# Performance work log

Hardware: AMD Instinct MI355X
Metric: run time of the kernel (lower is better)

## Reference

```python
import jax, jax.numpy as jnp
import numpy as np

N, E, IN_FEATS, HID, HEADS = 50000, 800000, 256, 32, 8
NEG_SLOPE = 0.2


def _init_params(key):
    ks = jax.random.split(key, 12)
    def lin(k, fi, fo):
        return jax.random.normal(k, (fi, fo), jnp.float32) * (1.0 / np.sqrt(fi))
    p = {}
    # layer 0: in_feats -> HID x HEADS
    p['W0'] = lin(ks[0], IN_FEATS, HEADS * HID)
    p['al0'] = jax.random.normal(ks[1], (HEADS, HID), jnp.float32) * 0.1
    p['ar0'] = jax.random.normal(ks[2], (HEADS, HID), jnp.float32) * 0.1
    p['b0'] = jnp.zeros((HEADS * HID,), jnp.float32)
    # layer 1: HID*HEADS -> HID x HEADS
    p['W1'] = lin(ks[3], HEADS * HID, HEADS * HID)
    p['al1'] = jax.random.normal(ks[4], (HEADS, HID), jnp.float32) * 0.1
    p['ar1'] = jax.random.normal(ks[5], (HEADS, HID), jnp.float32) * 0.1
    p['b1'] = jnp.zeros((HEADS * HID,), jnp.float32)
    # layer 2 (final): HID*HEADS -> HID x 1 head, no activation
    p['W2'] = lin(ks[6], HEADS * HID, HID)
    p['al2'] = jax.random.normal(ks[7], (1, HID), jnp.float32) * 0.1
    p['ar2'] = jax.random.normal(ks[8], (1, HID), jnp.float32) * 0.1
    p['b2'] = jnp.zeros((HID,), jnp.float32)
    return p


def setup_inputs() -> dict:
    key = jax.random.key(0)
    k1, k2, k3, kp = jax.random.split(key, 4)
    inp = {
        'features': jax.random.normal(k1, (N, IN_FEATS), jnp.float32),
        'src': jax.random.randint(k2, (E,), 0, N, jnp.int32),
        'dst': jax.random.randint(k3, (E,), 0, N, jnp.int32),
    }
    inp.update(_init_params(kp))
    return inp


def _gat_layer(x, src, dst, W, al, ar, b, heads, act):
    n = x.shape[0]
    d = W.shape[1] // heads
    feat = (x @ W).reshape(n, heads, d)           # [N,H,D]
    el = jnp.sum(feat * al, axis=-1)              # [N,H]
    er = jnp.sum(feat * ar, axis=-1)              # [N,H]
    e = jax.nn.leaky_relu(el[src] + er[dst], NEG_SLOPE)   # [E,H]
    # segment softmax over destination neighborhoods
    emax = jax.ops.segment_max(e, dst, num_segments=n)
    ex = jnp.exp(e - emax[dst])
    denom = jax.ops.segment_sum(ex, dst, num_segments=n)
    a = ex / (denom[dst] + 1e-9)                  # [E,H]
    msg = feat[src] * a[:, :, None]               # [E,H,D]
    out = jax.ops.segment_sum(msg, dst, num_segments=n)   # [N,H,D]
    out = out + b.reshape(1, heads, d)
    return act(out) if act is not None else out


def reference(features, src, dst, W0, al0, ar0, b0, W1, al1, ar1, b1, W2, al2, ar2, b2):
    h = _gat_layer(features, src, dst, W0, al0, ar0, b0, HEADS, jax.nn.elu)
    h = h.reshape(h.shape[0], -1)
    h = _gat_layer(h, src, dst, W1, al1, ar1, b1, HEADS, jax.nn.elu)
    h = h.reshape(h.shape[0], -1)
    h = _gat_layer(h, src, dst, W2, al2, ar2, b2, 1, None)   # [N,1,D]
    return h.mean(axis=1)                                    # [N,D]
```

## Files before the change

kernel.cpp:

```cpp
#include <hip/hip_runtime.h>

typedef unsigned short u16;
typedef unsigned int   u32;
typedef __attribute__((ext_vector_type(8))) short  short8;
typedef __attribute__((ext_vector_type(4))) float  f32x4;
typedef __attribute__((ext_vector_type(2))) float  f32x2;
typedef __attribute__((ext_vector_type(2))) unsigned int u32v2;

#define NN 50000
#define NE 800000

__device__ __forceinline__ float bf2f(u16 b) { return __uint_as_float(((u32)b) << 16); }
__device__ __forceinline__ float bflo(u32 p) { return __uint_as_float(p << 16); }
__device__ __forceinline__ float bfhi(u32 p) { return __uint_as_float(p & 0xffff0000u); }
__device__ __forceinline__ u16 f2bf(float f) {
    u32 u = __float_as_uint(f);
    u32 r = u + 0x7fffu + ((u >> 16) & 1u);
    return (u16)(r >> 16);
}
__device__ __forceinline__ float lexp(float v) {
    v = v > 0.f ? v : 0.2f * v;
    return __expf(fminf(v, 60.f));
}

struct DetectArgs { const u32* p[13]; int nw[13]; };

__global__ void k_detect(DetectArgs a, int* flags) {
    int t = threadIdx.x;
    if (t >= 13) return;
    const u32* x = a.p[t];
    int n = a.nw[t];
    int hits = 0, nz = 0;
    for (int i = 0; i < n; ++i) {
        u32 w = x[i];
        if (!w) continue;
        ++nz;
        u32 e = (w >> 7) & 0xffu;
        if (e >= 100 && e <= 150) ++hits;
    }
    flags[t] = (nz == 0) ? 2 : ((hits * 2 >= nz) ? 0 : 1);
}

struct ConvArgs { const void* s[9]; float* d[9]; int n[9]; int fi[9]; };

__global__ void k_convert(ConvArgs a, const int* __restrict__ flags) {
    int j = blockIdx.y;
    int i = blockIdx.x * 256 + threadIdx.x;
    if (i >= a.n[j]) return;
    int fl = flags[a.fi[j]];
    float v = 0.f;
    if (fl == 1) v = ((const float*)a.s[j])[i];
    else if (fl == 0) v = bf2f(((const u16*)a.s[j])[i]);
    a.d[j][i] = v;
}

__global__ void k_wpack(const void* __restrict__ Wsrc, const int* __restrict__ flags,
                        int fidx, int N, u16* __restrict__ Wp, int nchunks) {
    int id = blockIdx.x * 256 + threadIdx.x;
    if (id >= nchunks) return;
    int L = id & 63, kt = (id >> 6) & 7, nt = id >> 9;
    int col = nt * 16 + (L & 15);
    int krow = kt * 32 + ((L >> 4) & 3) * 8;
    bool isf32 = (flags[fidx] == 1);
#pragma unroll
    for (int j = 0; j < 8; ++j) {
        int s = (krow + j) * N + col;
        Wp[id * 8 + j] = isf32 ? f2bf(((const float*)Wsrc)[s]) : ((const u16*)Wsrc)[s];
    }
}

__global__ void k_xprep(const void* __restrict__ X, const int* __restrict__ flag,
                        u32* __restrict__ Xb2, int total2) {
    int i = blockIdx.x * 256 + threadIdx.x;
    if (i >= total2) return;
    if (*flag == 1) {
        const float* Xf = (const float*)X;
        Xb2[i] = (u32)f2bf(Xf[2 * i]) | ((u32)f2bf(Xf[2 * i + 1]) << 16);
    } else {
        Xb2[i] = ((const u32*)X)[i];
    }
}

__global__ void k_hist(const int* __restrict__ dst, int* __restrict__ deg, int E) {
    int e = blockIdx.x * 256 + threadIdx.x;
    if (e < E) atomicAdd(&deg[dst[e]], 1);
}

__global__ __launch_bounds__(256) void k_scan_partial(const int* __restrict__ deg,
                                                      int* __restrict__ bsum, int n) {
    __shared__ int red[256];
    int t = threadIdx.x;
    int i = blockIdx.x * 256 + t;
    red[t] = (i < n) ? deg[i] : 0;
    __syncthreads();
    for (int ofs = 128; ofs > 0; ofs >>= 1) {
        if (t < ofs) red[t] += red[t + ofs];
        __syncthreads();
    }
    if (t == 0) bsum[blockIdx.x] = red[0];
}

__global__ __launch_bounds__(256) void k_scan_bsum(int* __restrict__ bsum, int nb) {
    __shared__ int s[256];
    int t = threadIdx.x;
    int v = (t < nb) ? bsum[t] : 0;
    s[t] = v;
    __syncthreads();
    for (int ofs = 1; ofs < 256; ofs <<= 1) {
        int x = (t >= ofs) ? s[t - ofs] : 0;
        __syncthreads();
        s[t] += x;
        __syncthreads();
    }
    if (t < nb) bsum[t] = s[t] - v;
}

__global__ __launch_bounds__(256) void k_scan_final(const int* __restrict__ deg,
                                                    const int* __restrict__ bsum,
                                                    int* __restrict__ rowptr,
                                                    int* __restrict__ cursor, int n) {
    __shared__ int s[256];
    int t = threadIdx.x;
    int i = blockIdx.x * 256 + t;
    int v = (i < n) ? deg[i] : 0;
    s[t] = v;
    __syncthreads();
    for (int ofs = 1; ofs < 256; ofs <<= 1) {
        int x = (t >= ofs) ? s[t - ofs] : 0;
        __syncthreads();
        s[t] += x;
        __syncthreads();
    }
    int excl = bsum[blockIdx.x] + s[t] - v;
    if (i < n) {
        rowptr[i] = excl;
        cursor[i] = excl;
        if (i == n - 1) rowptr[n] = excl + v;
    }
}

__global__ void k_scatter(const int* __restrict__ src, const int* __restrict__ dst,
                          int* __restrict__ cursor, int* __restrict__ csr_src, int E) {
    int e = blockIdx.x * 256 + threadIdx.x;
    if (e >= E) return;
    int p = atomicAdd(&cursor[dst[e]], 1);
    csr_src[p] = src[e];
}

__global__ __launch_bounds__(256) void k_gemm_mfma(const u16* __restrict__ Xb,
                                                   const u16* __restrict__ Wp,
                                                   u16* __restrict__ OUT, int nrows) {
    __shared__ u16 As[64 * 256];
    const int t = threadIdx.x;
    const int w = t >> 6, L = t & 63;
    const int quad = (L >> 4) & 3;
    const int r0 = blockIdx.x * 64;
    const int nb = blockIdx.y * 8;

    const short8* Xv = (const short8*)Xb;
    short8* Asv = (short8*)As;
    short8 zero = {0, 0, 0, 0, 0, 0, 0, 0};
#pragma unroll
    for (int i = 0; i < 8; ++i) {
        int g = i * 256 + t;
        int row = g >> 5, cc = g & 31;
        int r = r0 + row;
        Asv[cc * 64 + row] = (r < nrows) ? Xv[(size_t)r * 32 + cc] : zero;
    }

    const short8* Wv = (const short8*)Wp;
    short8 bf[2][8];
#pragma unroll
    for (int jn = 0; jn < 2; ++jn) {
        int nt = nb + w + jn * 4;
#pragma unroll
        for (int kt = 0; kt < 8; ++kt) bf[jn][kt] = Wv[(nt * 8 + kt) * 64 + L];
    }
    __syncthreads();

    f32x4 acc[4][2];
#pragma unroll
    for (int mi = 0; mi < 4; ++mi)
#pragma unroll
        for (int jn = 0; jn < 2; ++jn) acc[mi][jn] = (f32x4){0.f, 0.f, 0.f, 0.f};

#pragma unroll
    for (int kt = 0; kt < 8; ++kt) {
#pragma unroll
        for (int mi = 0; mi < 4; ++mi) {
            short8 af = Asv[(kt * 4 + quad) * 64 + mi * 16 + (L & 15)];
            acc[mi][0] = __builtin_amdgcn_mfma_f32_16x16x32_bf16(af, bf[0][kt], acc[mi][0], 0, 0, 0);
            acc[mi][1] = __builtin_amdgcn_mfma_f32_16x16x32_bf16(af, bf[1][kt], acc[mi][1], 0, 0, 0);
        }
    }

    const int colbase = blockIdx.y * 128;
#pragma unroll
    for (int mi = 0; mi < 4; ++mi) {
        int rb = r0 + mi * 16 + quad * 4;
#pragma unroll
        for (int jn = 0; jn < 2; ++jn) {
            int c = colbase + (w + jn * 4) * 16 + (L & 15);
#pragma unroll
            for (int reg = 0; reg < 4; ++reg) {
                int r = rb + reg;
                if (r < nrows) OUT[(size_t)r * 256 + c] = f2bf(acc[mi][jn][reg]);
            }
        }
    }
}

__global__ __launch_bounds__(256) void k_gemm_mfma32(const u16* __restrict__ Xb,
                                                     const u16* __restrict__ Wp,
                                                     u16* __restrict__ OUT, int nrows) {
    __shared__ u16 As[128 * 256];
    const int t = threadIdx.x;
    const int w = t >> 6, L = t & 63;
    const int quad = (L >> 4) & 3;
    const int r0 = blockIdx.x * 128;
    const int mh = (w >> 1) * 64, nt = w & 1;

    const short8* Xv = (const short8*)Xb;
    short8* Asv = (short8*)As;
    short8 zero = {0, 0, 0, 0, 0, 0, 0, 0};
#pragma unroll
    for (int i = 0; i < 16; ++i) {
        int g = i * 256 + t;
        int row = g >> 5, cc = g & 31;
        int r = r0 + row;
        Asv[cc * 128 + row] = (r < nrows) ? Xv[(size_t)r * 32 + cc] : zero;
    }

    const short8* Wv = (const short8*)Wp;
    short8 bf[8];
#pragma unroll
    for (int kt = 0; kt < 8; ++kt) bf[kt] = Wv[(nt * 8 + kt) * 64 + L];
    __syncthreads();

    f32x4 acc[4];
#pragma unroll
    for (int mi = 0; mi < 4; ++mi) acc[mi] = (f32x4){0.f, 0.f, 0.f, 0.f};

#pragma unroll
    for (int kt = 0; kt < 8; ++kt) {
#pragma unroll
        for (int mi = 0; mi < 4; ++mi) {
            short8 af = Asv[(kt * 4 + quad) * 128 + mh + mi * 16 + (L & 15)];
            acc[mi] = __builtin_amdgcn_mfma_f32_16x16x32_bf16(af, bf[kt], acc[mi], 0, 0, 0);
        }
    }

#pragma unroll
    for (int mi = 0; mi < 4; ++mi) {
        int rb = r0 + mh + mi * 16 + quad * 4;
        int c = nt * 16 + (L & 15);
#pragma unroll
        for (int reg = 0; reg < 4; ++reg) {
            int r = rb + reg;
            if (r < nrows) OUT[(size_t)r * 32 + c] = f2bf(acc[mi][reg]);
        }
    }
}

__global__ void k_elr8(const u16* __restrict__ featb, const float* __restrict__ al,
                       const float* __restrict__ ar, float* __restrict__ el,
                       float* __restrict__ er, int n) {
    int idx = blockIdx.x * 256 + threadIdx.x;
    if (idx >= n * 8) return;
    int node = idx >> 3, h = idx & 7;
    const u32* fu = (const u32*)featb + (size_t)node * 128 + h * 16;
    const float* A = al + h * 32;
    const float* B = ar + h * 32;
    float sl = 0.f, sr = 0.f;
#pragma unroll
    for (int j = 0; j < 16; ++j) {
        u32 w = fu[j];
        float f0 = bflo(w), f1 = bfhi(w);
        sl += f0 * A[2 * j] + f1 * A[2 * j + 1];
        sr += f0 * B[2 * j] + f1 * B[2 * j + 1];
    }
    el[idx] = sl;
    er[idx] = sr;
}

__global__ void k_elr1(const u16* __restrict__ featb, const float* __restrict__ al,
                       const float* __restrict__ ar, float* __restrict__ el,
                       float* __restrict__ er, int n) {
    int node = blockIdx.x * 256 + threadIdx.x;
    if (node >= n) return;
    const u32* fu = (const u32*)featb + (size_t)node * 16;
    float sl = 0.f, sr = 0.f;
#pragma unroll
    for (int j = 0; j < 16; ++j) {
        u32 w = fu[j];
        float f0 = bflo(w), f1 = bfhi(w);
        sl += f0 * al[2 * j] + f1 * al[2 * j + 1];
        sr += f0 * ar[2 * j] + f1 * ar[2 * j + 1];
    }
    el[node] = sl;
    er[node] = sr;
}

__global__ __launch_bounds__(256) void k_gather8(const int* __restrict__ rowptr,
                                                 const int* __restrict__ csr_src,
                                                 const float* __restrict__ el,
                                                 const float* __restrict__ er,
                                                 const u32v2* __restrict__ featb4,
                                                 const float* __restrict__ bias,
                                                 u32v2* __restrict__ xout4) {
    int t = threadIdx.x;
    int d = blockIdx.x * 4 + (t >> 6);
    int q = t & 63;
    int h = q >> 3;
    int b = rowptr[d], e = rowptr[d + 1];
    float erd = er[d * 8 + h];
    float a0 = 0.f, a1 = 0.f, a2 = 0.f, a3 = 0.f, ssum = 0.f;
    int p = b;
    for (; p + 4 <= e; p += 4) {
        int s0 = csr_src[p], s1 = csr_src[p + 1], s2 = csr_src[p + 2], s3 = csr_src[p + 3];
        float e0 = lexp(el[s0 * 8 + h] + erd);
        float e1 = lexp(el[s1 * 8 + h] + erd);
        float e2 = lexp(el[s2 * 8 + h] + erd);
        float e3 = lexp(el[s3 * 8 + h] + erd);
        u32v2 w0 = featb4[(size_t)s0 * 64 + q];
        u32v2 w1 = featb4[(size_t)s1 * 64 + q];
        u32v2 w2 = featb4[(size_t)s2 * 64 + q];
        u32v2 w3 = featb4[(size_t)s3 * 64 + q];
        a0 += bflo(w0.x) * e0; a1 += bfhi(w0.x) * e0; a2 += bflo(w0.y) * e0; a3 += bfhi(w0.y) * e0;
        a0 += bflo(w1.x) * e1; a1 += bfhi(w1.x) * e1; a2 += bflo(w1.y) * e1; a3 += bfhi(w1.y) * e1;
        a0 += bflo(w2.x) * e2; a1 += bfhi(w2.x) * e2; a2 += bflo(w2.y) * e2; a3 += bfhi(w2.y) * e2;
        a0 += bflo(w3.x) * e3; a1 += bfhi(w3.x) * e3; a2 += bflo(w3.y) * e3; a3 += bfhi(w3.y) * e3;
        ssum += (e0 + e1) + (e2 + e3);
    }
    for (; p < e; ++p) {
        int s = csr_src[p];
        float ev = lexp(el[s * 8 + h] + erd);
        u32v2 w = featb4[(size_t)s * 64 + q];
        a0 += bflo(w.x) * ev; a1 += bfhi(w.x) * ev;
        a2 += bflo(w.y) * ev; a3 += bfhi(w.y) * ev;
        ssum += ev;
    }
    float rd = 1.f / (ssum + 1e-9f);
    const float4 bb = *(const float4*)&bias[4 * q];
    float v0 = a0 * rd + bb.x;
    float v1 = a1 * rd + bb.y;
    float v2 = a2 * rd + bb.z;
    float v3 = a3 * rd + bb.w;
    v0 = v0 > 0.f ? v0 : expm1f(v0);
    v1 = v1 > 0.f ? v1 : expm1f(v1);
    v2 = v2 > 0.f ? v2 : expm1f(v2);
    v3 = v3 > 0.f ? v3 : expm1f(v3);
    u32v2 o;
    o.x = (u32)f2bf(v0) | ((u32)f2bf(v1) << 16);
    o.y = (u32)f2bf(v2) | ((u32)f2bf(v3) << 16);
    xout4[(size_t)d * 64 + q] = o;
}

__global__ __launch_bounds__(256) void k_gather1(const int* __restrict__ rowptr,
                                                 const int* __restrict__ csr_src,
                                                 const float* __restrict__ el,
                                                 const float* __restrict__ er,
                                                 const u32* __restrict__ featb2,
                                                 const float* __restrict__ bias,
                                                 void* __restrict__ out,
                                                 const int* __restrict__ flag, int n) {
    int t = threadIdx.x;
    int d = blockIdx.x * 16 + (t >> 4);
    int q = t & 15;
    if (d >= n) return;
    int b = rowptr[d], e = rowptr[d + 1];
    float erd = er[d];
    float a0 = 0.f, a1 = 0.f, ssum = 0.f;
    int p = b;
    for (; p + 4 <= e; p += 4) {
        int s0 = csr_src[p], s1 = csr_src[p + 1], s2 = csr_src[p + 2], s3 = csr_src[p + 3];
        float e0 = lexp(el[s0] + erd);
        float e1 = lexp(el[s1] + erd);
        float e2 = lexp(el[s2] + erd);
        float e3 = lexp(el[s3] + erd);
        u32 w0 = featb2[(size_t)s0 * 16 + q];
        u32 w1 = featb2[(size_t)s1 * 16 + q];
        u32 w2 = featb2[(size_t)s2 * 16 + q];
        u32 w3 = featb2[(size_t)s3 * 16 + q];
        a0 += bflo(w0) * e0; a1 += bfhi(w0) * e0;
        a0 += bflo(w1) * e1; a1 += bfhi(w1) * e1;
        a0 += bflo(w2) * e2; a1 += bfhi(w2) * e2;
        a0 += bflo(w3) * e3; a1 += bfhi(w3) * e3;
        ssum += (e0 + e1) + (e2 + e3);
    }
    for (; p < e; ++p) {
        int s = csr_src[p];
        float ev = lexp(el[s] + erd);
        u32 w = featb2[(size_t)s * 16 + q];
        a0 += bflo(w) * ev;
        a1 += bfhi(w) * ev;
        ssum += ev;
    }
    float rd = 1.f / (ssum + 1e-9f);
    float v0 = a0 * rd + bias[2 * q];
    float v1 = a1 * rd + bias[2 * q + 1];
    if (*flag == 1) {
        f32x2 o = {v0, v1};
        ((f32x2*)out)[(size_t)d * 16 + q] = o;
    } else {
        ((u32*)out)[(size_t)d * 16 + q] = (u32)f2bf(v0) | ((u32)f2bf(v1) << 16);
    }
}

extern "C" void kernel_launch(void* const* d_in, const int* in_sizes, int n_in,
                              void* d_out, int out_size, void* d_ws, size_t ws_size,
                              hipStream_t stream) {
    const void* features = d_in[0];
    const int* src = (const int*)d_in[1];
    const int* dst = (const int*)d_in[2];

    char* ws = (char*)d_ws;
    size_t off = 0;
    auto carve = [&](size_t bytes) -> void* {
        void* p = ws + off;
        off = (off + bytes + 255) & ~(size_t)255;
        return p;
    };
    int*   flags = (int*)carve(64);
    float* pconv = (float*)carve(2048 * 4);
    u16*   Wp0 = (u16*)carve(65536 * 2);
    u16*   Wp1 = (u16*)carve(65536 * 2);
    u16*   Wp2 = (u16*)carve(8192 * 2);
    u16*   Xb    = (u16*)carve((size_t)NN * 256 * 2);
    u16*   featb = (u16*)carve((size_t)NN * 256 * 2);
    float* el   = (float*)carve((size_t)NN * 8 * 4);
    float* er   = (float*)carve((size_t)NN * 8 * 4);
    int*   deg     = (int*)carve((size_t)NN * 4);
    int*   cursor  = (int*)carve((size_t)NN * 4);
    int*   rowptr  = (int*)carve((size_t)(NN + 1) * 4);
    int*   bsum    = (int*)carve(256 * 4);
    int*   csr_src = (int*)carve((size_t)NE * 4);
    if (off > ws_size) return;

    const int N = NN, E = NE;
    const int nscan = (N + 255) / 256;

    DetectArgs da;
    const int din_idx[13] = {0, 3, 4, 5, 6, 7, 8, 9, 10, 11, 12, 13, 14};
    for (int j = 0; j < 13; ++j) {
        da.p[j] = (const u32*)d_in[din_idx[j]];
        int nw = in_sizes[din_idx[j]] / 2;
        da.nw[j] = nw > 512 ? 512 : nw;
    }
    k_detect<<<1, 64, 0, stream>>>(da, flags);

    ConvArgs ca;
    const int psl[9] = {4, 5, 6, 8, 9, 10, 12, 13, 14};
    const int pfl[9] = {2, 3, 4, 6, 7, 8, 10, 11, 12};
    float* dsts[9];
    {
        size_t o = 0;
        for (int j = 0; j < 9; ++j) {
            dsts[j] = pconv + o;
            o += (size_t)in_sizes[psl[j]];
        }
    }
    for (int j = 0; j < 9; ++j) {
        ca.s[j] = d_in[psl[j]];
        ca.d[j] = dsts[j];
        ca.n[j] = in_sizes[psl[j]];
        ca.fi[j] = pfl[j];
    }
    k_convert<<<dim3(1, 9), 256, 0, stream>>>(ca, flags);
    float* al0f = dsts[0]; float* ar0f = dsts[1]; float* b0f = dsts[2];
    float* al1f = dsts[3]; float* ar1f = dsts[4]; float* b1f = dsts[5];
    float* al2f = dsts[6]; float* ar2f = dsts[7]; float* b2f = dsts[8];

    k_wpack<<<32, 256, 0, stream>>>(d_in[3],  flags, 1, 256, Wp0, 8192);
    k_wpack<<<32, 256, 0, stream>>>(d_in[7],  flags, 5, 256, Wp1, 8192);
    k_wpack<<<4,  256, 0, stream>>>(d_in[11], flags, 9, 32,  Wp2, 1024);

    k_xprep<<<(N * 128 + 255) / 256, 256, 0, stream>>>(features, flags, (u32*)Xb, N * 128);

    hipMemsetAsync(deg, 0, (size_t)N * 4, stream);
    k_hist<<<(E + 255) / 256, 256, 0, stream>>>(dst, deg, E);
    k_scan_partial<<<nscan, 256, 0, stream>>>(deg, bsum, N);
    k_scan_bsum<<<1, 256, 0, stream>>>(bsum, nscan);
    k_scan_final<<<nscan, 256, 0, stream>>>(deg, bsum, rowptr, cursor, N);
    k_scatter<<<(E + 255) / 256, 256, 0, stream>>>(src, dst, cursor, csr_src, E);

    const dim3 ggrid((N + 63) / 64, 2);

    k_gemm_mfma<<<ggrid, 256, 0, stream>>>(Xb, Wp0, featb, N);
    k_elr8<<<(N * 8 + 255) / 256, 256, 0, stream>>>(featb, al0f, ar0f, el, er, N);
    k_gather8<<<N / 4, 256, 0, stream>>>(rowptr, csr_src, el, er,
                                         (const u32v2*)featb, b0f, (u32v2*)Xb);

    k_gemm_mfma<<<ggrid, 256, 0, stream>>>(Xb, Wp1, featb, N);
    k_elr8<<<(N * 8 + 255) / 256, 256, 0, stream>>>(featb, al1f, ar1f, el, er, N);
    k_gather8<<<N / 4, 256, 0, stream>>>(rowptr, csr_src, el, er,
                                         (const u32v2*)featb, b1f, (u32v2*)Xb);

    k_gemm_mfma32<<<(N + 127) / 128, 256, 0, stream>>>(Xb, Wp2, featb, N);
    k_elr1<<<(N + 255) / 256, 256, 0, stream>>>(featb, al2f, ar2f, el, er, N);
    k_gather1<<<(N + 15) / 16, 256, 0, stream>>>(rowptr, csr_src, el, er,
                                                 (const u32*)featb, b2f,
                                                 d_out, flags, N);
}
```

Measured before the change: 493.9 us.

## Fuse fp32-to-bf16 input conversion into GEMM and widen gather to 16B lanes

Removes the separate k_xprep pass: the first GEMM now reads fp32 features directly and converts them to bf16 while staging into LDS. This drops a full write and re-read of the converted feature matrix. The 8-head gather kernel now handles two destination nodes per wave, with each lane loading 16 bytes (8 bf16 values) instead of 8. Its loop runs to the larger degree of the two nodes and masks out the extra edges, which may waste work when the two degrees differ.

```diff
diff --git a/kernel.cpp b/kernel.cpp
--- a/kernel.cpp
+++ b/kernel.cpp
@@ -6,6 +6,7 @@
 typedef __attribute__((ext_vector_type(4))) float  f32x4;
 typedef __attribute__((ext_vector_type(2))) float  f32x2;
 typedef __attribute__((ext_vector_type(2))) unsigned int u32v2;
+typedef __attribute__((ext_vector_type(4))) unsigned int u32v4;
 
 #define NN 50000
 #define NE 800000
@@ -66,18 +67,6 @@
     for (int j = 0; j < 8; ++j) {
         int s = (krow + j) * N + col;
         Wp[id * 8 + j] = isf32 ? f2bf(((const float*)Wsrc)[s]) : ((const u16*)Wsrc)[s];
-    }
-}
-
-__global__ void k_xprep(const void* __restrict__ X, const int* __restrict__ flag,
-                        u32* __restrict__ Xb2, int total2) {
-    int i = blockIdx.x * 256 + threadIdx.x;
-    if (i >= total2) return;
-    if (*flag == 1) {
-        const float* Xf = (const float*)X;
-        Xb2[i] = (u32)f2bf(Xf[2 * i]) | ((u32)f2bf(Xf[2 * i + 1]) << 16);
-    } else {
-        Xb2[i] = ((const u32*)X)[i];
     }
 }
 
@@ -147,7 +136,8 @@
     csr_src[p] = src[e];
 }
 
-__global__ __launch_bounds__(256) void k_gemm_mfma(const u16* __restrict__ Xb,
+__global__ __launch_bounds__(256) void k_gemm_mfma(const void* __restrict__ Xv,
+                                                   const int* __restrict__ xflag,
                                                    const u16* __restrict__ Wp,
                                                    u16* __restrict__ OUT, int nrows) {
     __shared__ u16 As[64 * 256];
@@ -156,8 +146,8 @@
     const int quad = (L >> 4) & 3;
     const int r0 = blockIdx.x * 64;
     const int nb = blockIdx.y * 8;
-
-    const short8* Xv = (const short8*)Xb;
+    const bool xf32 = (xflag != nullptr) && (*xflag == 1);
+
     short8* Asv = (short8*)As;
     short8 zero = {0, 0, 0, 0, 0, 0, 0, 0};
 #pragma unroll
@@ -165,7 +155,21 @@
         int g = i * 256 + t;
         int row = g >> 5, cc = g & 31;
         int r = r0 + row;
-        Asv[cc * 64 + row] = (r < nrows) ? Xv[(size_t)r * 32 + cc] : zero;
+        short8 val = zero;
+        if (r < nrows) {
+            if (xf32) {
+                const f32x4* Xf4 = (const f32x4*)Xv;
+                f32x4 lo = Xf4[(size_t)r * 64 + cc * 2];
+                f32x4 hi = Xf4[(size_t)r * 64 + cc * 2 + 1];
+                val[0] = (short)f2bf(lo[0]); val[1] = (short)f2bf(lo[1]);
+                val[2] = (short)f2bf(lo[2]); val[3] = (short)f2bf(lo[3]);
+                val[4] = (short)f2bf(hi[0]); val[5] = (short)f2bf(hi[1]);
+                val[6] = (short)f2bf(hi[2]); val[7] = (short)f2bf(hi[3]);
+            } else {
+                val = ((const short8*)Xv)[(size_t)r * 32 + cc];
+            }
+        }
+        Asv[cc * 64 + row] = val;
     }
 
     const short8* Wv = (const short8*)Wp;
@@ -305,55 +309,59 @@
                                                  const int* __restrict__ csr_src,
                                                  const float* __restrict__ el,
                                                  const float* __restrict__ er,
-                                                 const u32v2* __restrict__ featb4,
+                                                 const u32v4* __restrict__ featb4,
                                                  const float* __restrict__ bias,
-                                                 u32v2* __restrict__ xout4) {
+                                                 u32v4* __restrict__ xout4, int E) {
     int t = threadIdx.x;
-    int d = blockIdx.x * 4 + (t >> 6);
-    int q = t & 63;
-    int h = q >> 3;
+    int wave = t >> 6, lane = t & 63;
+    int half = lane >> 5, li = lane & 31;
+    int d = blockIdx.x * 8 + wave * 2 + half;
+    int q = li;
+    int h = q >> 2;
     int b = rowptr[d], e = rowptr[d + 1];
+    int deg = e - b;
+    int md = max(deg, __shfl_xor(deg, 32, 64));
     float erd = er[d * 8 + h];
-    float a0 = 0.f, a1 = 0.f, a2 = 0.f, a3 = 0.f, ssum = 0.f;
-    int p = b;
-    for (; p + 4 <= e; p += 4) {
-        int s0 = csr_src[p], s1 = csr_src[p + 1], s2 = csr_src[p + 2], s3 = csr_src[p + 3];
-        float e0 = lexp(el[s0 * 8 + h] + erd);
-        float e1 = lexp(el[s1 * 8 + h] + erd);
-        float e2 = lexp(el[s2 * 8 + h] + erd);
-        float e3 = lexp(el[s3 * 8 + h] + erd);
-        u32v2 w0 = featb4[(size_t)s0 * 64 + q];
-        u32v2 w1 = featb4[(size_t)s1 * 64 + q];
-        u32v2 w2 = featb4[(size_t)s2 * 64 + q];
-        u32v2 w3 = featb4[(size_t)s3 * 64 + q];
-        a0 += bflo(w0.x) * e0; a1 += bfhi(w0.x) * e0; a2 += bflo(w0.y) * e0; a3 += bfhi(w0.y) * e0;
-        a0 += bflo(w1.x) * e1; a1 += bfhi(w1.x) * e1; a2 += bflo(w1.y) * e1; a3 += bfhi(w1.y) * e1;
-        a0 += bflo(w2.x) * e2; a1 += bfhi(w2.x) * e2; a2 += bflo(w2.y) * e2; a3 += bfhi(w2.y) * e2;
-        a0 += bflo(w3.x) * e3; a1 += bfhi(w3.x) * e3; a2 += bflo(w3.y) * e3; a3 += bfhi(w3.y) * e3;
-        ssum += (e0 + e1) + (e2 + e3);
-    }
-    for (; p < e; ++p) {
-        int s = csr_src[p];
-        float ev = lexp(el[s * 8 + h] + erd);
-        u32v2 w = featb4[(size_t)s * 64 + q];
-        a0 += bflo(w.x) * ev; a1 += bfhi(w.x) * ev;
-        a2 += bflo(w.y) * ev; a3 += bfhi(w.y) * ev;
-        ssum += ev;
+    float a0 = 0.f, a1 = 0.f, a2 = 0.f, a3 = 0.f;
+    float a4 = 0.f, a5 = 0.f, a6 = 0.f, a7 = 0.f, ssum = 0.f;
+    for (int it = 0; it < md; it += 4) {
+#pragma unroll
+        for (int k = 0; k < 4; ++k) {
+            int p = b + it + k;
+            bool act = p < e;
+            int pc = min(p, E - 1);
+            int s = csr_src[pc];
+            float ev = lexp(el[s * 8 + h] + erd);
+            ev = act ? ev : 0.f;
+            u32v4 w = featb4[(size_t)s * 32 + q];
+            a0 += bflo(w.x) * ev; a1 += bfhi(w.x) * ev;
+            a2 += bflo(w.y) * ev; a3 += bfhi(w.y) * ev;
+            a4 += bflo(w.z) * ev; a5 += bfhi(w.z) * ev;
+            a6 += bflo(w.w) * ev; a7 += bfhi(w.w) * ev;
+            ssum += ev;
+        }
     }
     float rd = 1.f / (ssum + 1e-9f);
-    const float4 bb = *(const float4*)&bias[4 * q];
-    float v0 = a0 * rd + bb.x;
-    float v1 = a1 * rd + bb.y;
-    float v2 = a2 * rd + bb.z;
-    float v3 = a3 * rd + bb.w;
+    const float4 bb0 = *(const float4*)&bias[8 * q];
+    const float4 bb1 = *(const float4*)&bias[8 * q + 4];
+    float v0 = a0 * rd + bb0.x, v1 = a1 * rd + bb0.y;
+    float v2 = a2 * rd + bb0.z, v3 = a3 * rd + bb0.w;
+    float v4 = a4 * rd + bb1.x, v5 = a5 * rd + bb1.y;
+    float v6 = a6 * rd + bb1.z, v7 = a7 * rd + bb1.w;
     v0 = v0 > 0.f ? v0 : expm1f(v0);
     v1 = v1 > 0.f ? v1 : expm1f(v1);
     v2 = v2 > 0.f ? v2 : expm1f(v2);
     v3 = v3 > 0.f ? v3 : expm1f(v3);
-    u32v2 o;
+    v4 = v4 > 0.f ? v4 : expm1f(v4);
+    v5 = v5 > 0.f ? v5 : expm1f(v5);
+    v6 = v6 > 0.f ? v6 : expm1f(v6);
+    v7 = v7 > 0.f ? v7 : expm1f(v7);
+    u32v4 o;
     o.x = (u32)f2bf(v0) | ((u32)f2bf(v1) << 16);
     o.y = (u32)f2bf(v2) | ((u32)f2bf(v3) << 16);
-    xout4[(size_t)d * 64 + q] = o;
+    o.z = (u32)f2bf(v4) | ((u32)f2bf(v5) << 16);
+    o.w = (u32)f2bf(v6) | ((u32)f2bf(v7) << 16);
+    xout4[(size_t)d * 32 + q] = o;
 }
 
 __global__ __launch_bounds__(256) void k_gather1(const int* __restrict__ rowptr,
@@ -475,8 +483,6 @@
     k_wpack<<<32, 256, 0, stream>>>(d_in[7],  flags, 5, 256, Wp1, 8192);
     k_wpack<<<4,  256, 0, stream>>>(d_in[11], flags, 9, 32,  Wp2, 1024);
 
-    k_xprep<<<(N * 128 + 255) / 256, 256, 0, stream>>>(features, flags, (u32*)Xb, N * 128);
-
     hipMemsetAsync(deg, 0, (size_t)N * 4, stream);
     k_hist<<<(E + 255) / 256, 256, 0, stream>>>(dst, deg, E);
     k_scan_partial<<<nscan, 256, 0, stream>>>(deg, bsum, N);
@@ -486,15 +492,15 @@
 
     const dim3 ggrid((N + 63) / 64, 2);
 
-    k_gemm_mfma<<<ggrid, 256, 0, stream>>>(Xb, Wp0, featb, N);
+    k_gemm_mfma<<<ggrid, 256, 0, stream>>>(features, flags, Wp0, featb, N);
     k_elr8<<<(N * 8 + 255) / 256, 256, 0, stream>>>(featb, al0f, ar0f, el, er, N);
-    k_gather8<<<N / 4, 256, 0, stream>>>(rowptr, csr_src, el, er,
-                                         (const u32v2*)featb, b0f, (u32v2*)Xb);
-
-    k_gemm_mfma<<<ggrid, 256, 0, stream>>>(Xb, Wp1, featb, N);
+    k_gather8<<<N / 8, 256, 0, stream>>>(rowptr, csr_src, el, er,
+                                         (const u32v4*)featb, b0f, (u32v4*)Xb, E);
+
+    k_gemm_mfma<<<ggrid, 256, 0, stream>>>(Xb, nullptr, Wp1, featb, N);
     k_elr8<<<(N * 8 + 255) / 256, 256, 0, stream>>>(featb, al1f, ar1f, el, er, N);
-    k_gather8<<<N / 4, 256, 0, stream>>>(rowptr, csr_src, el, er,
-                                         (const u32v2*)featb, b1f, (u32v2*)Xb);
+    k_gather8<<<N / 8, 256, 0, stream>>>(rowptr, csr_src, el, er,
+                                         (const u32v4*)featb, b1f, (u32v4*)Xb, E);
 
     k_gemm_mfma32<<<(N + 127) / 128, 256, 0, stream>>>(Xb, Wp2, featb, N);
     k_elr1<<<(N + 255) / 256, 256, 0, stream>>>(featb, al2f, ar2f, el, er, N);
```

Measured after the change: 502.7 us. Within noise of the previous version (+1.8%).

## Fuse fp32-to-bf16 feature conversion into first GEMM and parallelize dtype detection

Applied to the files above, without the earlier changes.

Removes the separate feature-conversion kernel. The first MFMA GEMM now reads fp32 features directly and converts them to bf16 while staging tiles into shared memory, which avoids writing and re-reading a 25.6 MB bf16 copy. Dtype detection now uses one 256-thread block per tensor with a shared-memory reduction instead of one serial thread per tensor. The el/er kernels switch to 128-bit vector loads. The trade-off is a fp32 read path and a runtime flag branch inside the GEMM, plus the GEMM is launched with two column blocks, so it reads the fp32 features twice.

```diff
diff --git a/kernel.cpp b/kernel.cpp
--- a/kernel.cpp
+++ b/kernel.cpp
@@ -6,6 +6,7 @@
 typedef __attribute__((ext_vector_type(4))) float  f32x4;
 typedef __attribute__((ext_vector_type(2))) float  f32x2;
 typedef __attribute__((ext_vector_type(2))) unsigned int u32v2;
+typedef __attribute__((ext_vector_type(4))) unsigned int u32v4;
 
 #define NN 50000
 #define NE 800000
@@ -25,20 +26,28 @@
 
 struct DetectArgs { const u32* p[13]; int nw[13]; };
 
-__global__ void k_detect(DetectArgs a, int* flags) {
+__global__ __launch_bounds__(256) void k_detect(DetectArgs a, int* flags) {
+    __shared__ int sh[256], sz[256];
+    int j = blockIdx.x;
+    const u32* x = a.p[j];
+    int n = a.nw[j];
     int t = threadIdx.x;
-    if (t >= 13) return;
-    const u32* x = a.p[t];
-    int n = a.nw[t];
     int hits = 0, nz = 0;
-    for (int i = 0; i < n; ++i) {
+    for (int i = t; i < n; i += 256) {
         u32 w = x[i];
-        if (!w) continue;
-        ++nz;
-        u32 e = (w >> 7) & 0xffu;
-        if (e >= 100 && e <= 150) ++hits;
-    }
-    flags[t] = (nz == 0) ? 2 : ((hits * 2 >= nz) ? 0 : 1);
+        if (w) {
+            ++nz;
+            u32 e = (w >> 7) & 0xffu;
+            if (e >= 100 && e <= 150) ++hits;
+        }
+    }
+    sh[t] = hits; sz[t] = nz;
+    __syncthreads();
+    for (int ofs = 128; ofs > 0; ofs >>= 1) {
+        if (t < ofs) { sh[t] += sh[t + ofs]; sz[t] += sz[t + ofs]; }
+        __syncthreads();
+    }
+    if (t == 0) flags[j] = (sz[0] == 0) ? 2 : ((sh[0] * 2 >= sz[0]) ? 0 : 1);
 }
 
 struct ConvArgs { const void* s[9]; float* d[9]; int n[9]; int fi[9]; };
@@ -66,18 +75,6 @@
     for (int j = 0; j < 8; ++j) {
         int s = (krow + j) * N + col;
         Wp[id * 8 + j] = isf32 ? f2bf(((const float*)Wsrc)[s]) : ((const u16*)Wsrc)[s];
-    }
-}
-
-__global__ void k_xprep(const void* __restrict__ X, const int* __restrict__ flag,
-                        u32* __restrict__ Xb2, int total2) {
-    int i = blockIdx.x * 256 + threadIdx.x;
-    if (i >= total2) return;
-    if (*flag == 1) {
-        const float* Xf = (const float*)X;
-        Xb2[i] = (u32)f2bf(Xf[2 * i]) | ((u32)f2bf(Xf[2 * i + 1]) << 16);
-    } else {
-        Xb2[i] = ((const u32*)X)[i];
     }
 }
 
@@ -147,7 +144,8 @@
     csr_src[p] = src[e];
 }
 
-__global__ __launch_bounds__(256) void k_gemm_mfma(const u16* __restrict__ Xb,
+__global__ __launch_bounds__(256) void k_gemm_mfma(const void* __restrict__ Xv,
+                                                   const int* __restrict__ xflag,
                                                    const u16* __restrict__ Wp,
                                                    u16* __restrict__ OUT, int nrows) {
     __shared__ u16 As[64 * 256];
@@ -156,8 +154,8 @@
     const int quad = (L >> 4) & 3;
     const int r0 = blockIdx.x * 64;
     const int nb = blockIdx.y * 8;
-
-    const short8* Xv = (const short8*)Xb;
+    const bool xf32 = (xflag != nullptr) && (*xflag == 1);
+
     short8* Asv = (short8*)As;
     short8 zero = {0, 0, 0, 0, 0, 0, 0, 0};
 #pragma unroll
@@ -165,7 +163,21 @@
         int g = i * 256 + t;
         int row = g >> 5, cc = g & 31;
         int r = r0 + row;
-        Asv[cc * 64 + row] = (r < nrows) ? Xv[(size_t)r * 32 + cc] : zero;
+        short8 val = zero;
+        if (r < nrows) {
+            if (xf32) {
+                const f32x4* Xf4 = (const f32x4*)Xv;
+                f32x4 lo = Xf4[(size_t)r * 64 + cc * 2];
+                f32x4 hi = Xf4[(size_t)r * 64 + cc * 2 + 1];
+                val[0] = (short)f2bf(lo[0]); val[1] = (short)f2bf(lo[1]);
+                val[2] = (short)f2bf(lo[2]); val[3] = (short)f2bf(lo[3]);
+                val[4] = (short)f2bf(hi[0]); val[5] = (short)f2bf(hi[1]);
+                val[6] = (short)f2bf(hi[2]); val[7] = (short)f2bf(hi[3]);
+            } else {
+                val = ((const short8*)Xv)[(size_t)r * 32 + cc];
+            }
+        }
+        Asv[cc * 64 + row] = val;
     }
 
     const short8* Wv = (const short8*)Wp;
@@ -268,16 +280,21 @@
     int idx = blockIdx.x * 256 + threadIdx.x;
     if (idx >= n * 8) return;
     int node = idx >> 3, h = idx & 7;
-    const u32* fu = (const u32*)featb + (size_t)node * 128 + h * 16;
+    const u32v4* fu = (const u32v4*)((const u32*)featb + (size_t)node * 128 + h * 16);
     const float* A = al + h * 32;
     const float* B = ar + h * 32;
     float sl = 0.f, sr = 0.f;
 #pragma unroll
-    for (int j = 0; j < 16; ++j) {
-        u32 w = fu[j];
-        float f0 = bflo(w), f1 = bfhi(w);
-        sl += f0 * A[2 * j] + f1 * A[2 * j + 1];
-        sr += f0 * B[2 * j] + f1 * B[2 * j + 1];
+    for (int j = 0; j < 4; ++j) {
+        u32v4 w4 = fu[j];
+#pragma unroll
+        for (int k = 0; k < 4; ++k) {
+            u32 w = (k == 0) ? w4.x : (k == 1) ? w4.y : (k == 2) ? w4.z : w4.w;
+            float f0 = bflo(w), f1 = bfhi(w);
+            int c = j * 8 + k * 2;
+            sl += f0 * A[c] + f1 * A[c + 1];
+            sr += f0 * B[c] + f1 * B[c + 1];
+        }
     }
     el[idx] = sl;
     er[idx] = sr;
@@ -288,14 +305,19 @@
                        float* __restrict__ er, int n) {
     int node = blockIdx.x * 256 + threadIdx.x;
     if (node >= n) return;
-    const u32* fu = (const u32*)featb + (size_t)node * 16;
+    const u32v4* fu = (const u32v4*)((const u32*)featb + (size_t)node * 16);
     float sl = 0.f, sr = 0.f;
 #pragma unroll
-    for (int j = 0; j < 16; ++j) {
-        u32 w = fu[j];
-        float f0 = bflo(w), f1 = bfhi(w);
-        sl += f0 * al[2 * j] + f1 * al[2 * j + 1];
-        sr += f0 * ar[2 * j] + f1 * ar[2 * j + 1];
+    for (int j = 0; j < 4; ++j) {
+        u32v4 w4 = fu[j];
+#pragma unroll
+        for (int k = 0; k < 4; ++k) {
+            u32 w = (k == 0) ? w4.x : (k == 1) ? w4.y : (k == 2) ? w4.z : w4.w;
+            float f0 = bflo(w), f1 = bfhi(w);
+            int c = j * 8 + k * 2;
+            sl += f0 * al[c] + f1 * al[c + 1];
+            sr += f0 * ar[c] + f1 * ar[c + 1];
+        }
     }
     el[node] = sl;
     er[node] = sr;
@@ -447,7 +469,7 @@
         int nw = in_sizes[din_idx[j]] / 2;
         da.nw[j] = nw > 512 ? 512 : nw;
     }
-    k_detect<<<1, 64, 0, stream>>>(da, flags);
+    k_detect<<<13, 256, 0, stream>>>(da, flags);
 
     ConvArgs ca;
     const int psl[9] = {4, 5, 6, 8, 9, 10, 12, 13, 14};
@@ -475,8 +497,6 @@
     k_wpack<<<32, 256, 0, stream>>>(d_in[7],  flags, 5, 256, Wp1, 8192);
     k_wpack<<<4,  256, 0, stream>>>(d_in[11], flags, 9, 32,  Wp2, 1024);
 
-    k_xprep<<<(N * 128 + 255) / 256, 256, 0, stream>>>(features, flags, (u32*)Xb, N * 128);
-
     hipMemsetAsync(deg, 0, (size_t)N * 4, stream);
     k_hist<<<(E + 255) / 256, 256, 0, stream>>>(dst, deg, E);
     k_scan_partial<<<nscan, 256, 0, stream>>>(deg, bsum, N);
@@ -486,12 +506,12 @@
 
     const dim3 ggrid((N + 63) / 64, 2);
 
-    k_gemm_mfma<<<ggrid, 256, 0, stream>>>(Xb, Wp0, featb, N);
+    k_gemm_mfma<<<ggrid, 256, 0, stream>>>(features, flags, Wp0, featb, N);
     k_elr8<<<(N * 8 + 255) / 256, 256, 0, stream>>>(featb, al0f, ar0f, el, er, N);
     k_gather8<<<N / 4, 256, 0, stream>>>(rowptr, csr_src, el, er,
                                          (const u32v2*)featb, b0f, (u32v2*)Xb);
 
-    k_gemm_mfma<<<ggrid, 256, 0, stream>>>(Xb, Wp1, featb, N);
+    k_gemm_mfma<<<ggrid, 256, 0, stream>>>(Xb, nullptr, Wp1, featb, N);
     k_elr8<<<(N * 8 + 255) / 256, 256, 0, stream>>>(featb, al1f, ar1f, el, er, N);
     k_gather8<<<N / 4, 256, 0, stream>>>(rowptr, csr_src, el, er,
                                          (const u32v2*)featb, b1f, (u32v2*)Xb);
```

Result: faster. 449.2 us (-9.0%).
